# Optimization experiments

Measured on AMD Instinct MI355X. Metric: run time of the kernel, lower is better.

Reference implementation:

```python
import jax, jax.numpy as jnp
from jax import lax
import numpy as np

# Config mirroring CSABlock(embed_dim=128, bs=8, heads=8, img_size=512, depth=2)
E = 128
BATCH = 8
HEADS = 8
RESO = 512 // 8      # 64
DEPTH = 2
SPLIT = 2            # split_size
C = 2 * E            # token dim = 256
C2 = C // 2          # per-branch dim
NH = HEADS // 2      # heads per branch
HID = 4 * C          # mlp hidden (mlp_ratio=4)
EPS = 1e-5


def setup_inputs() -> dict:
    key = jax.random.key(0)
    ks = iter(jax.random.split(key, 24))
    rn = lambda s, sd=0.02: jax.random.normal(next(ks), s, jnp.float32) * sd
    return {
        "x1": jax.random.normal(next(ks), (BATCH, E, RESO, RESO), jnp.float32),
        "x2": jax.random.normal(next(ks), (BATCH, E, RESO, RESO), jnp.float32),
        # conv_embed: Conv2d(C,C,3,1,1) + BatchNorm (eval) + LayerNorm
        "conv_w": rn((C, C, 3, 3)), "conv_b": jnp.zeros((C,), jnp.float32),
        "bn_g": jnp.ones((C,), jnp.float32), "bn_b": jnp.zeros((C,), jnp.float32),
        "bn_m": rn((C,), 0.1), "bn_v": jax.random.uniform(next(ks), (C,), jnp.float32) + 0.5,
        "ln0_g": jnp.ones((C,), jnp.float32), "ln0_b": jnp.zeros((C,), jnp.float32),
        # per-CSWinBlock params, stacked over DEPTH
        "n1_g": jnp.ones((DEPTH, C), jnp.float32), "n1_b": jnp.zeros((DEPTH, C), jnp.float32),
        "qkv_w": rn((DEPTH, C, 3 * C)),                       # Linear(dim, 3*dim, bias=False)
        "lepe_w": rn((DEPTH, 2, C2, 1, 3, 3)),                # depthwise get_v conv per branch
        "lepe_b": jnp.zeros((DEPTH, 2, C2), jnp.float32),
        "proj_w": rn((DEPTH, C, C)), "proj_b": jnp.zeros((DEPTH, C), jnp.float32),
        "n2_g": jnp.ones((DEPTH, C), jnp.float32), "n2_b": jnp.zeros((DEPTH, C), jnp.float32),
        "fc1_w": rn((DEPTH, C, HID)), "fc1_b": jnp.zeros((DEPTH, HID), jnp.float32),
        "fc2_w": rn((DEPTH, HID, C)), "fc2_b": jnp.zeros((DEPTH, C), jnp.float32),
    }


def _ln(x, g, b):
    mu = jnp.mean(x, -1, keepdims=True)
    var = jnp.mean((x - mu) ** 2, -1, keepdims=True)
    return (x - mu) * lax.rsqrt(var + EPS) * g + b


def _branch(q, k, v, Hs, Ws, dw_w, dw_b):
    """LePEAttention: cross-shaped stripe window attention with locally-enhanced PE.
    q,k,v: (B, L, C2); stripes of size Hs x Ws over a RESO x RESO grid."""
    B, L, c2 = q.shape
    H = W = RESO
    hd = c2 // NH
    scale = hd ** -0.5

    def to_win(t):  # (B,L,c2) -> (B*nW, NH, Hs*Ws, hd)
        t = t.reshape(B, H // Hs, Hs, W // Ws, Ws, c2)
        t = t.transpose(0, 1, 3, 2, 4, 5).reshape(-1, Hs * Ws, NH, hd)
        return t.transpose(0, 2, 1, 3)

    qw, kw = to_win(q), to_win(k)
    # v as per-window images for the depthwise LePE conv (padding is per-window)
    vimg = v.reshape(B, H // Hs, Hs, W // Ws, Ws, c2).transpose(0, 1, 3, 5, 2, 4)
    vimg = vimg.reshape(-1, c2, Hs, Ws)
    lepe = lax.conv_general_dilated(vimg, dw_w, (1, 1), [(1, 1), (1, 1)],
                                    dimension_numbers=("NCHW", "OIHW", "NCHW"),
                                    feature_group_count=c2) + dw_b[:, None, None]
    heads = lambda t: t.reshape(-1, NH, hd, Hs * Ws).transpose(0, 1, 3, 2)
    vw, lepe = heads(vimg), heads(lepe)

    attn = jax.nn.softmax(jnp.einsum("wnsd,wntd->wnst", qw * scale, kw), axis=-1)
    o = jnp.einsum("wnst,wntd->wnsd", attn, vw) + lepe      # (B*nW, NH, S, hd)
    # windows2img
    o = o.transpose(0, 2, 1, 3).reshape(B, H // Hs, W // Ws, Hs, Ws, c2)
    o = o.transpose(0, 1, 3, 2, 4, 5).reshape(B, L, c2)
    return o


def _forward(x1, x2, conv_w, conv_b, bn_g, bn_b, bn_m, bn_v, ln0_g, ln0_b,
             n1_g, n1_b, qkv_w, lepe_w, lepe_b, proj_w, proj_b,
             n2_g, n2_b, fc1_w, fc1_b, fc2_w, fc2_b):
    B, _, H, W = x1.shape
    t = jnp.concatenate([x1, x2], 1)                                   # (B, C, H, W)
    t = lax.conv_general_dilated(t, conv_w, (1, 1), [(1, 1), (1, 1)],
                                 dimension_numbers=("NCHW", "OIHW", "NCHW")) + conv_b[:, None, None]
    # BatchNorm2d in eval mode (running stats)
    t = (t - bn_m[:, None, None]) * lax.rsqrt(bn_v + EPS)[:, None, None] * bn_g[:, None, None] + bn_b[:, None, None]
    t = t.reshape(B, C, H * W).transpose(0, 2, 1)                      # b c h w -> b (h w) c
    t = _ln(t, ln0_g, ln0_b)

    for i in range(DEPTH):  # CSWinBlock x DEPTH
        img = _ln(t, n1_g[i], n1_b[i])
        qkv = (img @ qkv_w[i]).reshape(B, -1, 3, C)
        q, k, v = qkv[..., 0, :], qkv[..., 1, :], qkv[..., 2, :]
        # branch 0: horizontal stripes (H_sp=RESO, W_sp=SPLIT); branch 1: vertical
        xa = _branch(q[..., :C2], k[..., :C2], v[..., :C2], RESO, SPLIT, lepe_w[i, 0], lepe_b[i, 0])
        xb = _branch(q[..., C2:], k[..., C2:], v[..., C2:], SPLIT, RESO, lepe_w[i, 1], lepe_b[i, 1])
        att = jnp.concatenate([xa, xb], -1) @ proj_w[i] + proj_b[i]
        t = t + att
        y = _ln(t, n2_g[i], n2_b[i])
        t = t + (jax.nn.gelu(y @ fc1_w[i] + fc1_b[i], approximate=False) @ fc2_w[i] + fc2_b[i])

    x = t.transpose(0, 2, 1).reshape(B, C, H, W)
    return x[:, :E], x[:, E:]


def reference(x1, x2, conv_w, conv_b, bn_g, bn_b, bn_m, bn_v, ln0_g, ln0_b,
              n1_g, n1_b, qkv_w, lepe_w, lepe_b, proj_w, proj_b,
              n2_g, n2_b, fc1_w, fc1_b, fc2_w, fc2_b):
    return _forward(x1, x2, conv_w, conv_b, bn_g, bn_b, bn_m, bn_v, ln0_g, ln0_b,
                    n1_g, n1_b, qkv_w, lepe_w, lepe_b, proj_w, proj_b,
                    n2_g, n2_b, fc1_w, fc1_b, fc2_w, fc2_b)
```

## Files before the change

kernel.cpp:

```cpp
#include <hip/hip_runtime.h>
#include <hip/hip_bf16.h>

#define EPSV 1e-5f

using s8v = __attribute__((ext_vector_type(8))) short;
using f4v = __attribute__((ext_vector_type(4))) float;

__device__ __forceinline__ float bf2f(ushort u){
  union { unsigned int i; float f; } x; x.i = ((unsigned int)u)<<16; return x.f;
}
__device__ __forceinline__ ushort f2bf(float f){
  union { float f; unsigned int i; } x; x.f = f;
  unsigned int r = x.i + 0x7FFFu + ((x.i>>16)&1u);
  return (ushort)(r>>16);
}
__device__ __forceinline__ float wsum(float s){
  #pragma unroll
  for (int m=1;m<64;m<<=1) s += __shfl_xor(s, m);
  return s;
}
__device__ __forceinline__ float gelu_f(float t){
  return 0.5f*t*(1.0f + erff(t*0.70710678118654752f));
}

__device__ __forceinline__ void gload16(const void* g, void* l){
  __builtin_amdgcn_global_load_lds((__attribute__((address_space(1))) void*)g,
                                   (__attribute__((address_space(3))) void*)l, 16, 0, 0);
}

__global__ __launch_bounds__(256) void repack_in_k(const float* __restrict__ x1,
                                                   const float* __restrict__ x2,
                                                   ushort* __restrict__ Xin){
  __shared__ ushort tile[256][66];
  const int y = blockIdx.x, b = blockIdx.y, tid = threadIdx.x;
  const int xl = tid & 63, cq = tid >> 6;
  for (int it=0; it<64; it++){
    int ci = it*4 + cq;
    float v;
    if (ci < 128) v = x1[(((long)b*128 + ci)*64 + y)*64 + xl];
    else          v = x2[(((long)b*128 + (ci-128))*64 + y)*64 + xl];
    tile[ci][xl] = f2bf(v);
  }
  __syncthreads();
  for (int x=0; x<64; x++){
    Xin[(((long)b*66 + (y+1))*66 + (x+1))*256 + tid] = tile[tid][x];
  }
}

__global__ void prep_k(const float* __restrict__ conv_w, const float* __restrict__ qkv_w,
                       const float* __restrict__ proj_w, const float* __restrict__ fc1_w,
                       const float* __restrict__ fc2_w, const float* __restrict__ conv_b,
                       const float* __restrict__ bn_g, const float* __restrict__ bn_b,
                       const float* __restrict__ bn_m, const float* __restrict__ bn_v,
                       ushort* __restrict__ Wc, ushort* __restrict__ Wq, ushort* __restrict__ Wp,
                       ushort* __restrict__ W1, ushort* __restrict__ W2,
                       float* __restrict__ scv, float* __restrict__ shv)
{
  const long total = 589824L + 393216 + 131072 + 524288 + 524288 + 256;
  for (long idx = (long)blockIdx.x*256 + threadIdx.x; idx < total; idx += (long)gridDim.x*256){
    long e = idx;
    if (e < 589824){
      int co = (int)(e / 2304), kk = (int)(e % 2304);
      int dd = kk >> 8, ci = kk & 255;
      Wc[e] = f2bf(conv_w[((long)(co*256 + ci))*9 + dd]);
      continue;
    }
    e -= 589824;
    if (e < 393216){
      int l = (int)(e / 196608), r = (int)(e % 196608);
      int k = r / 768, n = r % 768;
      Wq[(long)l*196608 + (long)n*256 + k] = f2bf(qkv_w[(long)l*196608 + r]);
      continue;
    }
    e -= 393216;
    if (e < 131072){
      int l = (int)(e / 65536), r = (int)(e % 65536);
      int k = r >> 8, n = r & 255;
      Wp[(long)l*65536 + n*256 + k] = f2bf(proj_w[(long)l*65536 + r]);
      continue;
    }
    e -= 131072;
    if (e < 524288){
      int l = (int)(e / 262144), r = (int)(e % 262144);
      int k = r >> 10, n = r & 1023;
      W1[(long)l*262144 + (long)n*256 + k] = f2bf(fc1_w[(long)l*262144 + r]);
      continue;
    }
    e -= 524288;
    if (e < 524288){
      int l = (int)(e / 262144), r = (int)(e % 262144);
      int k = r >> 8, n = r & 255;
      W2[(long)l*262144 + (long)n*1024 + k] = f2bf(fc2_w[(long)l*262144 + r]);
      continue;
    }
    e -= 524288;
    {
      int n = (int)e;
      float s = bn_g[n] * rsqrtf(bn_v[n] + EPSV);
      scv[n] = s;
      shv[n] = (conv_b[n] - bn_m[n])*s + bn_b[n];
    }
  }
}

template<int EPI>
__global__ __launch_bounds__(256) void gemm_f(
    const ushort* __restrict__ A, const ushort* __restrict__ Xin,
    const ushort* __restrict__ Wt, const float* __restrict__ bias,
    const float* __restrict__ sc, const float* __restrict__ sh,
    float* __restrict__ T, const float* __restrict__ g1, const float* __restrict__ b1,
    const float* __restrict__ g2, const float* __restrict__ b2,
    ushort* __restrict__ Xb, float* __restrict__ dout, int K)
{
  constexpr bool CONVA = (EPI==0);
  __shared__ ushort SMEM[40960];
  const int tid = threadIdx.x, wid = tid>>6, lane = tid&63;
  const int m0 = blockIdx.x*64;
  const int l15 = lane&15, lg = lane>>4;
  const int rS = wid*8 + (lane>>3);
  const int cS = (((lane&7) ^ (lane>>3))*8);

  const ushort* pA[2];
  if (CONVA){
    #pragma unroll
    for (int j=0;j<2;j++){
      int t = m0 + j*32 + rS;
      int b = t>>12, y = (t>>6)&63, x = t&63;
      pA[j] = Xin + ((long)((b*66 + y+1)*66) + (x+1))*256 + cS;
    }
  } else {
    #pragma unroll
    for (int j=0;j<2;j++) pA[j] = A + (long)(m0 + j*32 + rS)*K + cS;
  }
  const ushort* pB[8];
  #pragma unroll
  for (int j=0;j<8;j++) pB[j] = Wt + (long)(j*32 + rS)*K + cS;

  auto stage = [&](int buf, int k0){
    ushort* AsB = SMEM + buf*20480;
    ushort* BsB = AsB + 4096;
    int koffA;
    if (CONVA){
      int dd = k0 >> 8;
      int dy = dd/3, dx = dd - dy*3;
      koffA = ((dy-1)*66 + (dx-1))*256 + (k0 & 255);
    } else koffA = k0;
    #pragma unroll
    for (int j=0;j<2;j++)
      gload16(pA[j] + koffA, (void*)&AsB[(j*256 + wid*64)*8]);
    #pragma unroll
    for (int j=0;j<8;j++)
      gload16(pB[j] + k0, (void*)&BsB[(j*256 + wid*64)*8]);
  };

  f4v acc[4][4] = {};

  int cur = 0;
  stage(0, 0);
  __syncthreads();
  for (int k0=0; k0<K; k0+=64){
    if (k0 + 64 < K) stage(cur^1, k0 + 64);
    const ushort* AsB = SMEM + cur*20480;
    const ushort* BsB = AsB + 4096;
    #pragma unroll
    for (int kk=0; kk<2; kk++){
      s8v a[4], b[4];
      const int kch = ((kk*4 + lg) ^ (l15 & 7))*8;
      #pragma unroll
      for (int mi=0;mi<4;mi++) a[mi] = *(const s8v*)&AsB[(mi*16 + l15)*64 + kch];
      #pragma unroll
      for (int ni=0;ni<4;ni++) b[ni] = *(const s8v*)&BsB[(wid*64 + ni*16 + l15)*64 + kch];
      #pragma unroll
      for (int mi=0;mi<4;mi++)
        #pragma unroll
        for (int ni=0;ni<4;ni++)
          acc[mi][ni] = __builtin_amdgcn_mfma_f32_16x16x32_bf16(a[mi], b[ni], acc[mi][ni], 0,0,0);
    }
    __syncthreads();
    cur ^= 1;
  }

  float* CT = (float*)SMEM;
  #pragma unroll
  for (int mi=0;mi<4;mi++)
    #pragma unroll
    for (int ni=0;ni<4;ni++)
      #pragma unroll
      for (int r=0;r<4;r++)
        CT[(mi*16 + lg*4 + r)*256 + wid*64 + ni*16 + l15] = acc[mi][ni][r];
  __syncthreads();

  const int c0 = lane*4;
  float4 scv4, shv4, bias4, g1v, b1v, g2v, b2v;
  if (EPI==0){
    scv4 = *(const float4*)&sc[c0]; shv4 = *(const float4*)&sh[c0];
    g1v = *(const float4*)&g1[c0];  b1v = *(const float4*)&b1[c0];
    g2v = *(const float4*)&g2[c0];  b2v = *(const float4*)&b2[c0];
  } else {
    bias4 = *(const float4*)&bias[c0];
    if (EPI==1){ g1v = *(const float4*)&g1[c0]; b1v = *(const float4*)&b1[c0]; }
  }

  for (int t=0; t<16; t++){
    const int r = wid*16 + t;
    const long gmr = m0 + r;
    float4 v = *(float4*)&CT[r*256 + c0];
    float4 t4;
    if (EPI==0){
      t4.x = v.x*scv4.x + shv4.x; t4.y = v.y*scv4.y + shv4.y;
      t4.z = v.z*scv4.z + shv4.z; t4.w = v.w*scv4.w + shv4.w;
    } else {
      float4 rv = *(float4*)&T[gmr*256 + c0];
      t4.x = rv.x + v.x + bias4.x; t4.y = rv.y + v.y + bias4.y;
      t4.z = rv.z + v.z + bias4.z; t4.w = rv.w + v.w + bias4.w;
    }
    if (EPI==3){
      *(float4*)&CT[r*256 + c0] = t4;
    } else {
      float mu = wsum(t4.x+t4.y+t4.z+t4.w) * (1.0f/256.0f);
      float d0=t4.x-mu, d1=t4.y-mu, d2=t4.z-mu, d3=t4.w-mu;
      float rs = rsqrtf(wsum(d0*d0+d1*d1+d2*d2+d3*d3)*(1.0f/256.0f) + EPSV);
      if (EPI==0){
        float u0 = d0*rs*g1v.x + b1v.x, u1 = d1*rs*g1v.y + b1v.y;
        float u2 = d2*rs*g1v.z + b1v.z, u3 = d3*rs*g1v.w + b1v.w;
        float4 u = {u0,u1,u2,u3};
        *(float4*)&T[gmr*256 + c0] = u;
        float mu2 = wsum(u0+u1+u2+u3) * (1.0f/256.0f);
        float e0=u0-mu2, e1=u1-mu2, e2=u2-mu2, e3=u3-mu2;
        float rs2 = rsqrtf(wsum(e0*e0+e1*e1+e2*e2+e3*e3)*(1.0f/256.0f) + EPSV);
        ushort4 o; o.x=f2bf(e0*rs2*g2v.x + b2v.x); o.y=f2bf(e1*rs2*g2v.y + b2v.y);
        o.z=f2bf(e2*rs2*g2v.z + b2v.z); o.w=f2bf(e3*rs2*g2v.w + b2v.w);
        *(ushort4*)&Xb[gmr*256 + c0] = o;
      } else {
        *(float4*)&T[gmr*256 + c0] = t4;
        ushort4 o; o.x=f2bf(d0*rs*g1v.x + b1v.x); o.y=f2bf(d1*rs*g1v.y + b1v.y);
        o.z=f2bf(d2*rs*g1v.z + b1v.z); o.w=f2bf(d3*rs*g1v.w + b1v.w);
        *(ushort4*)&Xb[gmr*256 + c0] = o;
      }
    }
  }

  if (EPI==3){
    __syncthreads();
    const int b_ = m0>>12, y_ = (m0>>6)&63;
    float* obase = dout + (long)b_*524288 + (long)y_*64;
    for (int it=0; it<64; it++){
      int e = it*256 + tid;
      int c = e>>6, x = e&63;
      obase[(long)(c>>7)*4194304 + (long)(c&127)*4096 + x] = CT[x*256 + c];
    }
  }
}

#define BM 128
#define BN 128
#define BK 64
__global__ __launch_bounds__(256) void gemm_fc1(
    const ushort* __restrict__ A,
    const ushort* __restrict__ Wt, const float* __restrict__ bias,
    ushort* __restrict__ outb, int N, int K)
{
  __shared__ ushort SMEM[BM*BK + BN*BK];
  ushort* As = SMEM;
  ushort* Bs = SMEM + BM*BK;
  const int tid = threadIdx.x, wid = tid>>6, lane = tid&63;
  const int m0 = blockIdx.x*BM, n0 = blockIdx.y*BN;
  const int wm = (wid>>1)*64, wn = (wid&1)*64;
  const int l15 = lane&15, lg = lane>>4;

  const int rA = wid*32 + (lane>>3);
  const int cS = (((lane&7) ^ (lane>>3))*8);
  const ushort* pA[4];
  #pragma unroll
  for (int j=0;j<4;j++) pA[j] = A + (long)(m0 + rA + j*8)*K + cS;
  const ushort* pB[4];
  #pragma unroll
  for (int j=0;j<4;j++) pB[j] = Wt + (long)(n0 + rA + j*8)*K + cS;

  f4v acc[4][4] = {};

  for (int k0=0; k0<K; k0+=BK){
    #pragma unroll
    for (int j=0;j<4;j++){
      gload16(pA[j] + k0, (void*)&As[(wid*32 + j*8)*BK]);
      gload16(pB[j] + k0, (void*)&Bs[(wid*32 + j*8)*BK]);
    }
    __syncthreads();
    #pragma unroll
    for (int kk=0; kk<2; kk++){
      s8v a[4], b[4];
      const int kch = ((kk*4 + lg) ^ (l15 & 7))*8;
      #pragma unroll
      for (int mi=0;mi<4;mi++) a[mi] = *(const s8v*)&As[(wm + mi*16 + l15)*BK + kch];
      #pragma unroll
      for (int ni=0;ni<4;ni++) b[ni] = *(const s8v*)&Bs[(wn + ni*16 + l15)*BK + kch];
      #pragma unroll
      for (int mi=0;mi<4;mi++)
        #pragma unroll
        for (int ni=0;ni<4;ni++)
          acc[mi][ni] = __builtin_amdgcn_mfma_f32_16x16x32_bf16(a[mi], b[ni], acc[mi][ni], 0,0,0);
    }
    __syncthreads();
  }

  float* CT = (float*)SMEM;
  #pragma unroll
  for (int p=0; p<2; p++){
    if ((wid>>1) == p){
      #pragma unroll
      for (int mi=0;mi<4;mi++)
        #pragma unroll
        for (int ni=0;ni<4;ni++)
          #pragma unroll
          for (int r=0;r<4;r++)
            CT[(mi*16 + lg*4 + r)*128 + wn + ni*16 + l15] = acc[mi][ni][r];
    }
    __syncthreads();
    #pragma unroll
    for (int it=0; it<8; it++){
      int e = it*256 + tid;
      int row = e >> 5;
      int c4 = e & 31;
      float4 v = *(float4*)&CT[row*128 + c4*4];
      int gm = m0 + p*64 + row;
      int gn = n0 + c4*4;
      float4 bv = *(const float4*)&bias[gn];
      float t0 = gelu_f(v.x + bv.x), t1 = gelu_f(v.y + bv.y);
      float t2 = gelu_f(v.z + bv.z), t3 = gelu_f(v.w + bv.w);
      ushort4 u; u.x=f2bf(t0); u.y=f2bf(t1); u.z=f2bf(t2); u.w=f2bf(t3);
      *(ushort4*)&outb[(long)gm*N + gn] = u;
    }
    __syncthreads();
  }
}

__global__ __launch_bounds__(256) void gemm_qkv(
    const ushort* __restrict__ A,
    const ushort* __restrict__ Wt,
    ushort* __restrict__ outb, int K)
{
  __shared__ ushort SMEM[BM*BK + BN*BK];
  ushort* As = SMEM;
  ushort* Bs = SMEM + BM*BK;
  const int tid = threadIdx.x, wid = tid>>6, lane = tid&63;
  const int m0 = blockIdx.x*BM, n0 = blockIdx.y*BN;
  const int wm = (wid>>1)*64, wn = (wid&1)*64;
  const int l15 = lane&15, lg = lane>>4;

  const int rA = wid*32 + (lane>>3);
  const int cS = (((lane&7) ^ (lane>>3))*8);
  const ushort* pA[4];
  #pragma unroll
  for (int j=0;j<4;j++) pA[j] = A + (long)(m0 + rA + j*8)*K + cS;
  const ushort* pB[4];
  #pragma unroll
  for (int j=0;j<4;j++) pB[j] = Wt + (long)(n0 + rA + j*8)*K + cS;

  f4v acc[4][4] = {};

  for (int k0=0; k0<K; k0+=BK){
    #pragma unroll
    for (int j=0;j<4;j++){
      gload16(pA[j] + k0, (void*)&As[(wid*32 + j*8)*BK]);
      gload16(pB[j] + k0, (void*)&Bs[(wid*32 + j*8)*BK]);
    }
    __syncthreads();
    #pragma unroll
    for (int kk=0; kk<2; kk++){
      s8v a[4], b[4];
      const int kch = ((kk*4 + lg) ^ (l15 & 7))*8;
      #pragma unroll
      for (int mi=0;mi<4;mi++) a[mi] = *(const s8v*)&As[(wm + mi*16 + l15)*BK + kch];
      #pragma unroll
      for (int ni=0;ni<4;ni++) b[ni] = *(const s8v*)&Bs[(wn + ni*16 + l15)*BK + kch];
      #pragma unroll
      for (int mi=0;mi<4;mi++)
        #pragma unroll
        for (int ni=0;ni<4;ni++)
          acc[mi][ni] = __builtin_amdgcn_mfma_f32_16x16x32_bf16(a[mi], b[ni], acc[mi][ni], 0,0,0);
    }
    __syncthreads();
  }

  ushort* CB = SMEM;
  #pragma unroll
  for (int ni=0;ni<4;ni++){
    const int c = wn + ni*16 + l15;
    const int j = c>>3, ce = c&7;
    #pragma unroll
    for (int mi=0;mi<4;mi++)
      #pragma unroll
      for (int r=0;r<4;r++){
        const int row = wm + mi*16 + lg*4 + r;
        CB[row*128 + (((j ^ (row&7))<<3) | ce)] = f2bf(acc[mi][ni][r]);
      }
  }
  __syncthreads();

  const int tile = n0 >> 8;
  const int brq  = (n0 >> 7) & 1;
  const int b_   = m0 >> 12;
  const int Y0   = (m0 >> 6) & 63;
  if (brq == 0){
    #pragma unroll
    for (int it=0; it<8; it++){
      int g = it*256 + tid;
      int seg = g >> 4, q = g & 15;
      int h = seg >> 5, wv = seg & 31;
      int svi = q >> 2, c8 = q & 3;
      int gm_local = (svi>>1)*64 + wv*2 + (svi&1);
      int jc = h*4 + c8;
      uint4 v = *(uint4*)&CB[gm_local*128 + ((jc ^ (gm_local&7))<<3)];
      long rowb = ((long)(tile*2)*4 + h)*32768L + ((long)b_*32 + wv)*128 + (Y0*2 + svi);
      *(uint4*)&outb[rowb*32 + c8*8] = v;
    }
  } else {
    const int wv = Y0 >> 1;
    #pragma unroll
    for (int it=0; it<8; it++){
      int g = it*256 + tid;
      int h = g >> 9, rem = g & 511, sv = rem >> 2, c8 = rem & 3;
      int jc = h*4 + c8;
      uint4 v = *(uint4*)&CB[sv*128 + ((jc ^ (sv&7))<<3)];
      long rowb = ((long)(tile*2 + 1)*4 + h)*32768L + ((long)b_*32 + wv)*128 + sv;
      *(uint4*)&outb[rowb*32 + c8*8] = v;
    }
  }
}

__global__ __launch_bounds__(256) void attn_k(
    const ushort* __restrict__ QKVw, ushort* __restrict__ ATT,
    const float* __restrict__ lepe_w, const float* __restrict__ lepe_b, int layer)
{
  __shared__ ushort q_lds[128][36];
  __shared__ ushort k_lds[128][36];
  __shared__ ushort vT[32][132];
  __shared__ float wl[32][9];
  __shared__ float bl[32];
  const int tid = threadIdx.x, wid = tid>>6, lane = tid&63;
  const int b = blockIdx.y;
  const int br = blockIdx.z;
  const int w = blockIdx.x>>2, h = blockIdx.x&3;
  const int choff = br*128 + h*32;
  const int l15 = lane&15, lg = lane>>4;

  const long rowbase = ((long)b*32 + w)*128;
  const ushort* qb = QKVw + (((long)(0*2+br)*4 + h)*32768L + rowbase)*32;
  const ushort* kb = QKVw + (((long)(1*2+br)*4 + h)*32768L + rowbase)*32;
  const ushort* vb = QKVw + (((long)(2*2+br)*4 + h)*32768L + rowbase)*32;

  for (int e = tid; e < 512; e += 256){
    int row = e>>2, c4 = (e&3)*8;
    *(uint4*)&q_lds[row][c4] = *(const uint4*)(qb + (long)e*8);
    *(uint4*)&k_lds[row][c4] = *(const uint4*)(kb + (long)e*8);
    uint4 val = *(const uint4*)(vb + (long)e*8);
    const ushort* u = (const ushort*)&val;
    #pragma unroll
    for (int jj=0;jj<8;jj++) vT[c4+jj][row] = u[jj];
  }
  for (int e = tid; e < 288; e += 256){
    int d = e/9, tap = e%9;
    wl[d][tap] = lepe_w[((long)((layer*2+br)*128 + h*32 + d))*9 + tap];
  }
  if (tid < 32) bl[tid] = lepe_b[(layer*2+br)*128 + h*32 + tid];
  __syncthreads();

  const int wrow = wid*32;
  const float scale = 0.17677669529663689f;
  const int srcE = (lane & 15) | ((lane & 16) << 1);
  const int srcO = srcE + 16;
  const bool hi = (lane >= 32);
  const int HsL = (br==0)?64:2, WsL = (br==0)?2:64;

  #pragma unroll
  for (int mi=0; mi<2; mi++){
    s8v aq = *(const s8v*)&q_lds[wrow + mi*16 + l15][lg*8];
    f4v S[8];
    #pragma unroll
    for (int ni=0; ni<8; ni++){
      s8v bk = *(const s8v*)&k_lds[ni*16 + l15][lg*8];
      f4v z = {0.f,0.f,0.f,0.f};
      S[ni] = __builtin_amdgcn_mfma_f32_16x16x32_bf16(bk, aq, z, 0,0,0);
    }
    float mx = -1e30f;
    #pragma unroll
    for (int ni=0; ni<8; ni++)
      #pragma unroll
      for (int r=0;r<4;r++){ S[ni][r] *= scale; mx = fmaxf(mx, S[ni][r]); }
    mx = fmaxf(mx, __shfl_xor(mx, 16));
    mx = fmaxf(mx, __shfl_xor(mx, 32));
    float sum = 0.f;
    #pragma unroll
    for (int ni=0; ni<8; ni++)
      #pragma unroll
      for (int r=0;r<4;r++){ S[ni][r] = __expf(S[ni][r]-mx); sum += S[ni][r]; }
    sum += __shfl_xor(sum, 16);
    sum += __shfl_xor(sum, 32);
    const float inv = 1.0f / sum;
    unsigned int Alo[8], Ahi[8];
    #pragma unroll
    for (int ni=0; ni<8; ni++){
      Alo[ni] = (unsigned)f2bf(S[ni][0]*inv) | ((unsigned)f2bf(S[ni][1]*inv)<<16);
      Ahi[ni] = (unsigned)f2bf(S[ni][2]*inv) | ((unsigned)f2bf(S[ni][3]*inv)<<16);
    }
    f4v acc2[2] = {{0.f,0.f,0.f,0.f},{0.f,0.f,0.f,0.f}};
    #pragma unroll
    for (int ks=0; ks<4; ks++){
      unsigned e0 = (unsigned)__shfl((int)Alo[2*ks],   srcE);
      unsigned e1 = (unsigned)__shfl((int)Ahi[2*ks],   srcE);
      unsigned e2 = (unsigned)__shfl((int)Alo[2*ks+1], srcE);
      unsigned e3 = (unsigned)__shfl((int)Ahi[2*ks+1], srcE);
      unsigned o0 = (unsigned)__shfl((int)Alo[2*ks],   srcO);
      unsigned o1 = (unsigned)__shfl((int)Ahi[2*ks],   srcO);
      unsigned o2 = (unsigned)__shfl((int)Alo[2*ks+1], srcO);
      unsigned o3 = (unsigned)__shfl((int)Ahi[2*ks+1], srcO);
      union { unsigned u[4]; s8v v; } ap;
      ap.u[0] = hi?e2:e0; ap.u[1] = hi?e3:e1; ap.u[2] = hi?o2:o0; ap.u[3] = hi?o3:o1;
      #pragma unroll
      for (int di=0; di<2; di++){
        s8v bv = *(const s8v*)&vT[di*16 + l15][ks*32 + lg*8];
        acc2[di] = __builtin_amdgcn_mfma_f32_16x16x32_bf16(ap.v, bv, acc2[di], 0,0,0);
      }
    }
    #pragma unroll
    for (int di=0; di<2; di++)
      #pragma unroll
      for (int r=0;r<4;r++){
        int s = wrow + mi*16 + lg*4 + r;
        int d = di*16 + l15;
        float v = acc2[di][r] + bl[d];
        int hs, ws2;
        if (br==0){ hs = s>>1; ws2 = s&1; }
        else      { hs = s>>6; ws2 = s&63; }
        #pragma unroll
        for (int a=-1;a<=1;a++)
          #pragma unroll
          for (int bb=-1;bb<=1;bb++){
            int h2 = hs+a, w2 = ws2+bb;
            if (h2>=0 && h2<HsL && w2>=0 && w2<WsL){
              int s2 = h2*WsL + w2;
              v += wl[d][(a+1)*3 + (bb+1)] * bf2f(vT[d][s2]);
            }
          }
        int y, x;
        if (br==0){ y = s>>1; x = (w<<1)|(s&1); }
        else      { y = (w<<1)|(s>>6); x = s&63; }
        long tok = ((long)b*64 + y)*64 + x;
        ATT[tok*256 + choff + d] = f2bf(v);
      }
  }
}

extern "C" void kernel_launch(void* const* d_in, const int* in_sizes, int n_in,
                              void* d_out, int out_size, void* d_ws, size_t ws_size,
                              hipStream_t stream)
{
  (void)in_sizes; (void)n_in; (void)out_size;
  const float* x1     = (const float*)d_in[0];
  const float* x2     = (const float*)d_in[1];
  const float* conv_w = (const float*)d_in[2];
  const float* conv_b = (const float*)d_in[3];
  const float* bn_g   = (const float*)d_in[4];
  const float* bn_b   = (const float*)d_in[5];
  const float* bn_m   = (const float*)d_in[6];
  const float* bn_v   = (const float*)d_in[7];
  const float* ln0_g  = (const float*)d_in[8];
  const float* ln0_b  = (const float*)d_in[9];
  const float* n1_g   = (const float*)d_in[10];
  const float* n1_b   = (const float*)d_in[11];
  const float* qkv_w  = (const float*)d_in[12];
  const float* lepe_w = (const float*)d_in[13];
  const float* lepe_b = (const float*)d_in[14];
  const float* proj_w = (const float*)d_in[15];
  const float* proj_b = (const float*)d_in[16];
  const float* n2_g   = (const float*)d_in[17];
  const float* n2_b   = (const float*)d_in[18];
  const float* fc1_w  = (const float*)d_in[19];
  const float* fc1_b  = (const float*)d_in[20];
  const float* fc2_w  = (const float*)d_in[21];
  const float* fc2_b  = (const float*)d_in[22];

  if (ws_size < 121767936ULL){
    hipMemsetAsync(d_out, 0, (size_t)out_size*4, stream);
    return;
  }

  char* ws = (char*)d_ws;
  ushort* Xin  = (ushort*)ws;
  ushort* QKVb = (ushort*)ws;
  ushort* H1b  = (ushort*)ws;
  ushort* ATTb = (ushort*)(ws + 50331648);
  float*  T    = (float*)(ws + 67108864);
  ushort* Xb   = (ushort*)(ws + 100663296);
  size_t off = 117440512;
  ushort* Wc   = (ushort*)(ws + off); off += 1179648;
  ushort* Wq   = (ushort*)(ws + off); off += 786432;
  ushort* Wp   = (ushort*)(ws + off); off += 262144;
  ushort* W1   = (ushort*)(ws + off); off += 1048576;
  ushort* W2   = (ushort*)(ws + off); off += 1048576;
  float*  scv  = (float*)(ws + off);  off += 1024;
  float*  shv  = (float*)(ws + off);  off += 1024;

  hipMemsetAsync(Xin, 0, (size_t)8*66*66*256*2, stream);
  repack_in_k<<<dim3(64,8), 256, 0, stream>>>(x1, x2, Xin);
  prep_k<<<1024, 256, 0, stream>>>(conv_w, qkv_w, proj_w, fc1_w, fc2_w,
                                   conv_b, bn_g, bn_b, bn_m, bn_v,
                                   Wc, Wq, Wp, W1, W2, scv, shv);

  gemm_f<0><<<512,256,0,stream>>>(nullptr, Xin, Wc, nullptr, scv, shv,
                                  T, ln0_g, ln0_b, n1_g, n1_b, Xb, nullptr, 2304);

  for (int i=0;i<2;i++){
    gemm_qkv<<<dim3(256,6),256,0,stream>>>(Xb, Wq + (long)i*196608, QKVb, 256);
    attn_k<<<dim3(128,8,2),256,0,stream>>>(QKVb, ATTb, lepe_w, lepe_b, i);
    gemm_f<1><<<512,256,0,stream>>>(ATTb, nullptr, Wp + (long)i*65536, proj_b + i*256,
                                    nullptr, nullptr, T, n2_g + i*256, n2_b + i*256,
                                    nullptr, nullptr, Xb, nullptr, 256);
    gemm_fc1<<<dim3(256,8),256,0,stream>>>(Xb, W1 + (long)i*262144, fc1_b + i*1024, H1b, 1024, 256);
    if (i == 0){
      gemm_f<1><<<512,256,0,stream>>>(H1b, nullptr, W2, fc2_b,
                                      nullptr, nullptr, T, n1_g + 256, n1_b + 256,
                                      nullptr, nullptr, Xb, nullptr, 1024);
    } else {
      gemm_f<3><<<512,256,0,stream>>>(H1b, nullptr, W2 + 262144, fc2_b + 256,
                                      nullptr, nullptr, T, nullptr, nullptr,
                                      nullptr, nullptr, nullptr, (float*)d_out, 1024);
    }
  }
}
```

Before: 446.0 us.

## Split conv GEMM from residual GEMMs and shrink LDS for single-buffered residual kernel

The shared templated GEMM is split into a dedicated conv-embed kernel and a residual-epilogue kernel. The residual kernel uses a single 40KB LDS buffer instead of an 80KB double buffer, and its epilogue drains in two 32-row halves so the fp32 staging tile fits in that smaller buffer. The aim is more resident blocks per CU and better latency hiding through occupancy. In exchange it loses the overlap of the next tile's global loads with MFMA work and adds extra barriers in the main loop and epilogue.

```diff
diff --git a/kernel.cpp b/kernel.cpp
--- a/kernel.cpp
+++ b/kernel.cpp
@@ -103,16 +103,14 @@
   }
 }
 
-template<int EPI>
-__global__ __launch_bounds__(256) void gemm_f(
-    const ushort* __restrict__ A, const ushort* __restrict__ Xin,
-    const ushort* __restrict__ Wt, const float* __restrict__ bias,
+__global__ __launch_bounds__(256) void gemm_conv(
+    const ushort* __restrict__ Xin, const ushort* __restrict__ Wt,
     const float* __restrict__ sc, const float* __restrict__ sh,
     float* __restrict__ T, const float* __restrict__ g1, const float* __restrict__ b1,
     const float* __restrict__ g2, const float* __restrict__ b2,
-    ushort* __restrict__ Xb, float* __restrict__ dout, int K)
+    ushort* __restrict__ Xb)
 {
-  constexpr bool CONVA = (EPI==0);
+  const int K = 2304;
   __shared__ ushort SMEM[40960];
   const int tid = threadIdx.x, wid = tid>>6, lane = tid&63;
   const int m0 = blockIdx.x*64;
@@ -121,16 +119,11 @@
   const int cS = (((lane&7) ^ (lane>>3))*8);
 
   const ushort* pA[2];
-  if (CONVA){
-    #pragma unroll
-    for (int j=0;j<2;j++){
-      int t = m0 + j*32 + rS;
-      int b = t>>12, y = (t>>6)&63, x = t&63;
-      pA[j] = Xin + ((long)((b*66 + y+1)*66) + (x+1))*256 + cS;
-    }
-  } else {
-    #pragma unroll
-    for (int j=0;j<2;j++) pA[j] = A + (long)(m0 + j*32 + rS)*K + cS;
+  #pragma unroll
+  for (int j=0;j<2;j++){
+    int t = m0 + j*32 + rS;
+    int b = t>>12, y = (t>>6)&63, x = t&63;
+    pA[j] = Xin + ((long)((b*66 + y+1)*66) + (x+1))*256 + cS;
   }
   const ushort* pB[8];
   #pragma unroll
@@ -139,12 +132,9 @@
   auto stage = [&](int buf, int k0){
     ushort* AsB = SMEM + buf*20480;
     ushort* BsB = AsB + 4096;
-    int koffA;
-    if (CONVA){
-      int dd = k0 >> 8;
-      int dy = dd/3, dx = dd - dy*3;
-      koffA = ((dy-1)*66 + (dx-1))*256 + (k0 & 255);
-    } else koffA = k0;
+    int dd = k0 >> 8;
+    int dy = dd/3, dx = dd - dy*3;
+    int koffA = ((dy-1)*66 + (dx-1))*256 + (k0 & 255);
     #pragma unroll
     for (int j=0;j<2;j++)
       gload16(pA[j] + koffA, (void*)&AsB[(j*256 + wid*64)*8]);
@@ -191,63 +181,128 @@
   __syncthreads();
 
   const int c0 = lane*4;
-  float4 scv4, shv4, bias4, g1v, b1v, g2v, b2v;
-  if (EPI==0){
-    scv4 = *(const float4*)&sc[c0]; shv4 = *(const float4*)&sh[c0];
-    g1v = *(const float4*)&g1[c0];  b1v = *(const float4*)&b1[c0];
-    g2v = *(const float4*)&g2[c0];  b2v = *(const float4*)&b2[c0];
-  } else {
-    bias4 = *(const float4*)&bias[c0];
-    if (EPI==1){ g1v = *(const float4*)&g1[c0]; b1v = *(const float4*)&b1[c0]; }
-  }
+  const float4 scv4 = *(const float4*)&sc[c0], shv4 = *(const float4*)&sh[c0];
+  const float4 g1v = *(const float4*)&g1[c0], b1v = *(const float4*)&b1[c0];
+  const float4 g2v = *(const float4*)&g2[c0], b2v = *(const float4*)&b2[c0];
 
   for (int t=0; t<16; t++){
     const int r = wid*16 + t;
     const long gmr = m0 + r;
     float4 v = *(float4*)&CT[r*256 + c0];
     float4 t4;
-    if (EPI==0){
-      t4.x = v.x*scv4.x + shv4.x; t4.y = v.y*scv4.y + shv4.y;
-      t4.z = v.z*scv4.z + shv4.z; t4.w = v.w*scv4.w + shv4.w;
-    } else {
+    t4.x = v.x*scv4.x + shv4.x; t4.y = v.y*scv4.y + shv4.y;
+    t4.z = v.z*scv4.z + shv4.z; t4.w = v.w*scv4.w + shv4.w;
+    float mu = wsum(t4.x+t4.y+t4.z+t4.w) * (1.0f/256.0f);
+    float d0=t4.x-mu, d1=t4.y-mu, d2=t4.z-mu, d3=t4.w-mu;
+    float rs = rsqrtf(wsum(d0*d0+d1*d1+d2*d2+d3*d3)*(1.0f/256.0f) + EPSV);
+    float u0 = d0*rs*g1v.x + b1v.x, u1 = d1*rs*g1v.y + b1v.y;
+    float u2 = d2*rs*g1v.z + b1v.z, u3 = d3*rs*g1v.w + b1v.w;
+    float4 u = {u0,u1,u2,u3};
+    *(float4*)&T[gmr*256 + c0] = u;
+    float mu2 = wsum(u0+u1+u2+u3) * (1.0f/256.0f);
+    float e0=u0-mu2, e1=u1-mu2, e2=u2-mu2, e3=u3-mu2;
+    float rs2 = rsqrtf(wsum(e0*e0+e1*e1+e2*e2+e3*e3)*(1.0f/256.0f) + EPSV);
+    ushort4 o; o.x=f2bf(e0*rs2*g2v.x + b2v.x); o.y=f2bf(e1*rs2*g2v.y + b2v.y);
+    o.z=f2bf(e2*rs2*g2v.z + b2v.z); o.w=f2bf(e3*rs2*g2v.w + b2v.w);
+    *(ushort4*)&Xb[gmr*256 + c0] = o;
+  }
+}
+
+template<int EPI>
+__global__ __launch_bounds__(256) void gemm_res(
+    const ushort* __restrict__ A, const ushort* __restrict__ Wt, const float* __restrict__ bias,
+    float* __restrict__ T, const float* __restrict__ g1, const float* __restrict__ b1,
+    ushort* __restrict__ Xb, float* __restrict__ dout, int K)
+{
+  __shared__ ushort SMEM[20480];
+  ushort* As = SMEM;
+  ushort* Bs = SMEM + 4096;
+  const int tid = threadIdx.x, wid = tid>>6, lane = tid&63;
+  const int m0 = blockIdx.x*64;
+  const int l15 = lane&15, lg = lane>>4;
+  const int rS = wid*8 + (lane>>3);
+  const int cS = (((lane&7) ^ (lane>>3))*8);
+
+  const ushort* pA[2];
+  #pragma unroll
+  for (int j=0;j<2;j++) pA[j] = A + (long)(m0 + j*32 + rS)*K + cS;
+  const ushort* pB[8];
+  #pragma unroll
+  for (int j=0;j<8;j++) pB[j] = Wt + (long)(j*32 + rS)*K + cS;
+
+  f4v acc[4][4] = {};
+
+  for (int k0=0; k0<K; k0+=64){
+    #pragma unroll
+    for (int j=0;j<2;j++)
+      gload16(pA[j] + k0, (void*)&As[(j*256 + wid*64)*8]);
+    #pragma unroll
+    for (int j=0;j<8;j++)
+      gload16(pB[j] + k0, (void*)&Bs[(j*256 + wid*64)*8]);
+    __syncthreads();
+    #pragma unroll
+    for (int kk=0; kk<2; kk++){
+      s8v a[4], b[4];
+      const int kch = ((kk*4 + lg) ^ (l15 & 7))*8;
+      #pragma unroll
+      for (int mi=0;mi<4;mi++) a[mi] = *(const s8v*)&As[(mi*16 + l15)*64 + kch];
+      #pragma unroll
+      for (int ni=0;ni<4;ni++) b[ni] = *(const s8v*)&Bs[(wid*64 + ni*16 + l15)*64 + kch];
+      #pragma unroll
+      for (int mi=0;mi<4;mi++)
+        #pragma unroll
+        for (int ni=0;ni<4;ni++)
+          acc[mi][ni] = __builtin_amdgcn_mfma_f32_16x16x32_bf16(a[mi], b[ni], acc[mi][ni], 0,0,0);
+    }
+    __syncthreads();
+  }
+
+  float* CT = (float*)SMEM;
+  const int c0 = lane*4;
+  const float4 bias4 = *(const float4*)&bias[c0];
+  float4 g1v, b1v;
+  if (EPI==1){ g1v = *(const float4*)&g1[c0]; b1v = *(const float4*)&b1[c0]; }
+  const int b_ = m0>>12, y_ = (m0>>6)&63;
+
+  #pragma unroll
+  for (int p=0; p<2; p++){
+    #pragma unroll
+    for (int mi=2*p; mi<2*p+2; mi++)
+      #pragma unroll
+      for (int ni=0;ni<4;ni++)
+        #pragma unroll
+        for (int r=0;r<4;r++)
+          CT[((mi-2*p)*16 + lg*4 + r)*256 + wid*64 + ni*16 + l15] = acc[mi][ni][r];
+    __syncthreads();
+    for (int t=0; t<8; t++){
+      const int r = wid*8 + t;
+      const long gmr = m0 + p*32 + r;
+      float4 v = *(float4*)&CT[r*256 + c0];
       float4 rv = *(float4*)&T[gmr*256 + c0];
+      float4 t4;
       t4.x = rv.x + v.x + bias4.x; t4.y = rv.y + v.y + bias4.y;
       t4.z = rv.z + v.z + bias4.z; t4.w = rv.w + v.w + bias4.w;
-    }
-    if (EPI==3){
-      *(float4*)&CT[r*256 + c0] = t4;
-    } else {
-      float mu = wsum(t4.x+t4.y+t4.z+t4.w) * (1.0f/256.0f);
-      float d0=t4.x-mu, d1=t4.y-mu, d2=t4.z-mu, d3=t4.w-mu;
-      float rs = rsqrtf(wsum(d0*d0+d1*d1+d2*d2+d3*d3)*(1.0f/256.0f) + EPSV);
-      if (EPI==0){
-        float u0 = d0*rs*g1v.x + b1v.x, u1 = d1*rs*g1v.y + b1v.y;
-        float u2 = d2*rs*g1v.z + b1v.z, u3 = d3*rs*g1v.w + b1v.w;
-        float4 u = {u0,u1,u2,u3};
-        *(float4*)&T[gmr*256 + c0] = u;
-        float mu2 = wsum(u0+u1+u2+u3) * (1.0f/256.0f);
-        float e0=u0-mu2, e1=u1-mu2, e2=u2-mu2, e3=u3-mu2;
-        float rs2 = rsqrtf(wsum(e0*e0+e1*e1+e2*e2+e3*e3)*(1.0f/256.0f) + EPSV);
-        ushort4 o; o.x=f2bf(e0*rs2*g2v.x + b2v.x); o.y=f2bf(e1*rs2*g2v.y + b2v.y);
-        o.z=f2bf(e2*rs2*g2v.z + b2v.z); o.w=f2bf(e3*rs2*g2v.w + b2v.w);
-        *(ushort4*)&Xb[gmr*256 + c0] = o;
+      if (EPI==3){
+        *(float4*)&CT[r*256 + c0] = t4;
       } else {
         *(float4*)&T[gmr*256 + c0] = t4;
+        float mu = wsum(t4.x+t4.y+t4.z+t4.w) * (1.0f/256.0f);
+        float d0=t4.x-mu, d1=t4.y-mu, d2=t4.z-mu, d3=t4.w-mu;
+        float rs = rsqrtf(wsum(d0*d0+d1*d1+d2*d2+d3*d3)*(1.0f/256.0f) + EPSV);
         ushort4 o; o.x=f2bf(d0*rs*g1v.x + b1v.x); o.y=f2bf(d1*rs*g1v.y + b1v.y);
         o.z=f2bf(d2*rs*g1v.z + b1v.z); o.w=f2bf(d3*rs*g1v.w + b1v.w);
         *(ushort4*)&Xb[gmr*256 + c0] = o;
       }
     }
-  }
-
-  if (EPI==3){
-    __syncthreads();
-    const int b_ = m0>>12, y_ = (m0>>6)&63;
-    float* obase = dout + (long)b_*524288 + (long)y_*64;
-    for (int it=0; it<64; it++){
-      int e = it*256 + tid;
-      int c = e>>6, x = e&63;
-      obase[(long)(c>>7)*4194304 + (long)(c&127)*4096 + x] = CT[x*256 + c];
+    __syncthreads();
+    if (EPI==3){
+      float* obase = dout + (long)b_*524288 + (long)y_*64 + p*32;
+      for (int it=0; it<32; it++){
+        int e = it*256 + tid;
+        int c = e>>5, xl = e&31;
+        obase[(long)(c>>7)*4194304 + (long)(c&127)*4096 + xl] = CT[xl*256 + c];
+      }
+      __syncthreads();
     }
   }
 }
@@ -607,24 +662,20 @@
                                    conv_b, bn_g, bn_b, bn_m, bn_v,
                                    Wc, Wq, Wp, W1, W2, scv, shv);
 
-  gemm_f<0><<<512,256,0,stream>>>(nullptr, Xin, Wc, nullptr, scv, shv,
-                                  T, ln0_g, ln0_b, n1_g, n1_b, Xb, nullptr, 2304);
+  gemm_conv<<<512,256,0,stream>>>(Xin, Wc, scv, shv, T, ln0_g, ln0_b, n1_g, n1_b, Xb);
 
   for (int i=0;i<2;i++){
     gemm_qkv<<<dim3(256,6),256,0,stream>>>(Xb, Wq + (long)i*196608, QKVb, 256);
     attn_k<<<dim3(128,8,2),256,0,stream>>>(QKVb, ATTb, lepe_w, lepe_b, i);
-    gemm_f<1><<<512,256,0,stream>>>(ATTb, nullptr, Wp + (long)i*65536, proj_b + i*256,
-                                    nullptr, nullptr, T, n2_g + i*256, n2_b + i*256,
-                                    nullptr, nullptr, Xb, nullptr, 256);
+    gemm_res<1><<<512,256,0,stream>>>(ATTb, Wp + (long)i*65536, proj_b + i*256,
+                                      T, n2_g + i*256, n2_b + i*256, Xb, nullptr, 256);
     gemm_fc1<<<dim3(256,8),256,0,stream>>>(Xb, W1 + (long)i*262144, fc1_b + i*1024, H1b, 1024, 256);
     if (i == 0){
-      gemm_f<1><<<512,256,0,stream>>>(H1b, nullptr, W2, fc2_b,
-                                      nullptr, nullptr, T, n1_g + 256, n1_b + 256,
-                                      nullptr, nullptr, Xb, nullptr, 1024);
+      gemm_res<1><<<512,256,0,stream>>>(H1b, W2, fc2_b,
+                                        T, n1_g + 256, n1_b + 256, Xb, nullptr, 1024);
     } else {
-      gemm_f<3><<<512,256,0,stream>>>(H1b, nullptr, W2 + 262144, fc2_b + 256,
-                                      nullptr, nullptr, T, nullptr, nullptr,
-                                      nullptr, nullptr, nullptr, (float*)d_out, 1024);
-    }
-  }
-}
+      gemm_res<3><<<512,256,0,stream>>>(H1b, W2 + 262144, fc2_b + 256,
+                                        T, nullptr, nullptr, nullptr, (float*)d_out, 1024);
+    }
+  }
+}
```

Measured after the change: 446.0 us. Within noise of the previous version (+0.0%).
